# Kernel optimization log

Hardware: AMD Instinct MI355X
Metric: run time of the kernel (lower is better)

## Reference

```python
import jax, jax.numpy as jnp
import numpy as np


def setup_inputs() -> dict:
    key = jax.random.key(0)
    k1, k2, k3, k4, k5 = jax.random.split(key, 5)
    NNZ = 1_600_000
    N, IN, OUT = 8192, 4096, 4096
    vals = jax.random.normal(k1, (NNZ,), dtype=jnp.float32)
    rows = jax.random.randint(k2, (NNZ,), 0, N, dtype=jnp.int32)
    cols = jax.random.randint(k3, (NNZ,), 0, IN, dtype=jnp.int32)
    # kaiming_uniform-ish init scale for weight, uniform bias
    bound_w = jnp.sqrt(1.0 / IN)
    weight = jax.random.uniform(k4, (OUT, IN), dtype=jnp.float32, minval=-bound_w, maxval=bound_w)
    bias = jax.random.uniform(k5, (OUT,), dtype=jnp.float32, minval=-bound_w, maxval=bound_w)
    return {"vals": vals, "rows": rows, "cols": cols, "weight": weight, "bias": bias, "n_rows": N}


def reference(vals, rows, cols, weight, bias, n_rows):
    """Sparse COO [n_rows, in_features] @ weight.T + bias (torch.sparse.addmm).

    Densify via scatter-add (COO semantics: duplicate indices accumulate),
    then a single dense GEMM which dominates the cost.
    """
    in_features = weight.shape[1]
    dense = jnp.zeros((n_rows, in_features), dtype=vals.dtype).at[rows, cols].add(vals)
    return dense @ weight.T + bias  # [n_rows, out_features]
```

## Files before the change

kernel.cpp:

```cpp
#include <hip/hip_runtime.h>

typedef __attribute__((ext_vector_type(8)))  __bf16 bf16x8;
typedef __attribute__((ext_vector_type(4)))  float  f32x4;
typedef __attribute__((ext_vector_type(8)))  unsigned short u16x8;

__device__ inline unsigned short f2bf(float f) {
    unsigned int u = __float_as_uint(f);
    u += 0x7FFFu + ((u >> 16) & 1u);
    return (unsigned short)(u >> 16);
}

__global__ __launch_bounds__(256) void scatter_bf16(
        const float* __restrict__ vals,
        const int* __restrict__ rows,
        const int* __restrict__ cols,
        unsigned short* __restrict__ Ab,
        int nnz, int in_f) {
    int i = blockIdx.x * blockDim.x + threadIdx.x;
    if (i >= nnz) return;
    float v = vals[i];
    size_t idx = (size_t)rows[i] * in_f + cols[i];
    unsigned int* word = (unsigned int*)(Ab + (idx & ~(size_t)1));
    unsigned int sh = (unsigned int)(idx & 1) * 16u;
    unsigned int old = *word, assumed;
    do {
        assumed = old;
        unsigned int cur = (assumed >> sh) & 0xFFFFu;
        float f = __uint_as_float(cur << 16) + v;
        unsigned int nb = f2bf(f);
        unsigned int repl = (assumed & ~(0xFFFFu << sh)) | (nb << sh);
        old = atomicCAS(word, assumed, repl);
    } while (old != assumed);
}

__global__ __launch_bounds__(256) void cvt_kernel(
        const float* __restrict__ src,
        unsigned short* __restrict__ dst,
        long n) {
    long i = ((long)blockIdx.x * blockDim.x + threadIdx.x) * 8;
    if (i + 8 <= n) {
        f32x4 a = *(const f32x4*)(src + i);
        f32x4 b = *(const f32x4*)(src + i + 4);
        u16x8 o;
        o[0] = f2bf(a[0]); o[1] = f2bf(a[1]); o[2] = f2bf(a[2]); o[3] = f2bf(a[3]);
        o[4] = f2bf(b[0]); o[5] = f2bf(b[1]); o[6] = f2bf(b[2]); o[7] = f2bf(b[3]);
        *(u16x8*)(dst + i) = o;
    }
}


__device__ __forceinline__ bf16x8 read_frag(const unsigned short* slab, int row, int g) {
    return *(const bf16x8*)(slab + row * 32 + ((g ^ (row & 3)) << 3));
}

__device__ __forceinline__ void stage_slab(const unsigned short* __restrict__ G,
                                           int grow0, int K, int kelem,
                                           unsigned short* slab, int tid) {
    const int lane = tid & 63, wv = tid >> 6;
    #pragma unroll
    for (int j = 0; j < 2; ++j) {
        int u = wv * 128 + j * 64 + lane;
        int row = u >> 2, slot = u & 3;
        const unsigned short* g = G + (size_t)(grow0 + row) * K
                                    + (kelem + ((slot ^ (row & 3)) << 3));
        unsigned short* l = slab + (wv * 128 + j * 64) * 8;
        __builtin_amdgcn_global_load_lds(
            (const __attribute__((address_space(1))) void*)g,
            (__attribute__((address_space(3))) void*)l, 16, 0, 0);
    }
}

__global__ __launch_bounds__(512, 2) void gemm_bt_bias(
    const unsigned short* __restrict__ A,
    const unsigned short* __restrict__ B,
    const float* __restrict__ bias,
    float* __restrict__ C,
    int M, int N, int K)
{
    __shared__ unsigned short sA[2][2][8192];
    __shared__ unsigned short sB[2][2][8192];

    const int tid  = threadIdx.x;
    const int lane = tid & 63;
    const int wave = tid >> 6;
    const int wm = (wave >> 2) * 128;
    const int wn = (wave & 3) * 64;
    const int r15 = lane & 15;
    const int g   = lane >> 4;

    const int nbx = gridDim.x;
    const int nwg = gridDim.x * gridDim.y;
    int flat = blockIdx.y * gridDim.x + blockIdx.x;
    int rid = (nwg & 7) ? flat : ((flat & 7) * (nwg >> 3) + (flat >> 3));
    const int bm = (rid / nbx) * 256;
    const int bn = (rid % nbx) * 256;

    f32x4 acc[8][4];
    #pragma unroll
    for (int i = 0; i < 8; ++i)
        #pragma unroll
        for (int jg = 0; jg < 4; ++jg)
            #pragma unroll
            for (int r = 0; r < 4; ++r) acc[i][jg][r] = 0.f;

    stage_slab(A, bm, K, 0,       &sA[0][0][0], tid);
    stage_slab(B, bn, K, 0,       &sB[0][0][0], tid);
    stage_slab(A, bm, K, 32,      &sA[0][1][0], tid);
    stage_slab(B, bn, K, 32,      &sB[0][1][0], tid);
    stage_slab(A, bm, K, 64,      &sA[1][0][0], tid);
    stage_slab(B, bn, K, 64,      &sB[1][0][0], tid);
    asm volatile("s_waitcnt vmcnt(8)" ::: "memory");
    __builtin_amdgcn_s_barrier();

    const int nt = K >> 6;
    for (int t = 0; t < nt; ++t) {
        const int cur = t & 1, nxt = cur ^ 1;
        const int t1k = ((t + 1 < nt) ? t + 1 : 0) << 6;
        const int t2k = ((t + 2 < nt) ? t + 2 : 0) << 6;
        const unsigned short* sAc0 = &sA[cur][0][0];
        const unsigned short* sAc1 = &sA[cur][1][0];
        const unsigned short* sBc0 = &sB[cur][0][0];
        const unsigned short* sBc1 = &sB[cur][1][0];

        bf16x8 a[8], b[2];

        #pragma unroll
        for (int i = 0; i < 8; ++i) a[i] = read_frag(sAc0, wm + i * 16 + r15, g);
        b[0] = read_frag(sBc0, wn + r15, g);
        b[1] = read_frag(sBc0, wn + 16 + r15, g);
        stage_slab(A, bm, K, t1k + 32, &sA[nxt][1][0], tid);
        __builtin_amdgcn_s_barrier();
        asm volatile("s_waitcnt lgkmcnt(0)" ::: "memory");
        __builtin_amdgcn_s_setprio(1);
        #pragma unroll
        for (int i = 0; i < 8; ++i) {
            acc[i][0] = __builtin_amdgcn_mfma_f32_16x16x32_bf16(a[i], b[0], acc[i][0], 0, 0, 0);
            acc[i][1] = __builtin_amdgcn_mfma_f32_16x16x32_bf16(a[i], b[1], acc[i][1], 0, 0, 0);
        }
        __builtin_amdgcn_s_setprio(0);
        __builtin_amdgcn_s_barrier();

        b[0] = read_frag(sBc0, wn + 32 + r15, g);
        b[1] = read_frag(sBc0, wn + 48 + r15, g);
        stage_slab(B, bn, K, t1k + 32, &sB[nxt][1][0], tid);
        __builtin_amdgcn_s_barrier();
        asm volatile("s_waitcnt lgkmcnt(0)" ::: "memory");
        __builtin_amdgcn_s_setprio(1);
        #pragma unroll
        for (int i = 0; i < 8; ++i) {
            acc[i][2] = __builtin_amdgcn_mfma_f32_16x16x32_bf16(a[i], b[0], acc[i][2], 0, 0, 0);
            acc[i][3] = __builtin_amdgcn_mfma_f32_16x16x32_bf16(a[i], b[1], acc[i][3], 0, 0, 0);
        }
        __builtin_amdgcn_s_setprio(0);
        asm volatile("s_waitcnt vmcnt(8)" ::: "memory");
        __builtin_amdgcn_s_barrier();

        #pragma unroll
        for (int i = 0; i < 8; ++i) a[i] = read_frag(sAc1, wm + i * 16 + r15, g);
        b[0] = read_frag(sBc1, wn + r15, g);
        b[1] = read_frag(sBc1, wn + 16 + r15, g);
        stage_slab(A, bm, K, t2k, &sA[cur][0][0], tid);
        __builtin_amdgcn_s_barrier();
        asm volatile("s_waitcnt lgkmcnt(0)" ::: "memory");
        __builtin_amdgcn_s_setprio(1);
        #pragma unroll
        for (int i = 0; i < 8; ++i) {
            acc[i][0] = __builtin_amdgcn_mfma_f32_16x16x32_bf16(a[i], b[0], acc[i][0], 0, 0, 0);
            acc[i][1] = __builtin_amdgcn_mfma_f32_16x16x32_bf16(a[i], b[1], acc[i][1], 0, 0, 0);
        }
        __builtin_amdgcn_s_setprio(0);
        __builtin_amdgcn_s_barrier();

        b[0] = read_frag(sBc1, wn + 32 + r15, g);
        b[1] = read_frag(sBc1, wn + 48 + r15, g);
        stage_slab(B, bn, K, t2k, &sB[cur][0][0], tid);
        __builtin_amdgcn_s_barrier();
        asm volatile("s_waitcnt lgkmcnt(0)" ::: "memory");
        __builtin_amdgcn_s_setprio(1);
        #pragma unroll
        for (int i = 0; i < 8; ++i) {
            acc[i][2] = __builtin_amdgcn_mfma_f32_16x16x32_bf16(a[i], b[0], acc[i][2], 0, 0, 0);
            acc[i][3] = __builtin_amdgcn_mfma_f32_16x16x32_bf16(a[i], b[1], acc[i][3], 0, 0, 0);
        }
        __builtin_amdgcn_s_setprio(0);
        asm volatile("s_waitcnt vmcnt(8)" ::: "memory");
        __builtin_amdgcn_s_barrier();
    }

    #pragma unroll
    for (int jg = 0; jg < 4; ++jg) {
        int col = bn + wn + jg * 16 + r15;
        float bv = bias[col];
        #pragma unroll
        for (int i = 0; i < 8; ++i) {
            int rbase = bm + wm + i * 16 + g * 4;
            #pragma unroll
            for (int r = 0; r < 4; ++r) {
                __builtin_nontemporal_store(acc[i][jg][r] + bv,
                                            &C[(size_t)(rbase + r) * N + col]);
            }
        }
    }
}

extern "C" void kernel_launch(void* const* d_in, const int* in_sizes, int n_in,
                              void* d_out, int out_size, void* d_ws, size_t ws_size,
                              hipStream_t stream) {
    const float* vals   = (const float*)d_in[0];
    const int*   rows   = (const int*)d_in[1];
    const int*   cols   = (const int*)d_in[2];
    const float* weight = (const float*)d_in[3];
    const float* bias   = (const float*)d_in[4];

    const int NNZ = in_sizes[0];
    const int OUT = in_sizes[4];
    const int IN  = in_sizes[3] / OUT;
    const int M   = out_size / OUT;

    unsigned short* Ab = (unsigned short*)d_ws;
    size_t abBytes = (size_t)M * IN * sizeof(unsigned short);
    unsigned short* Wb = (unsigned short*)((char*)d_ws + abBytes);

    hipMemsetAsync(Ab, 0, abBytes, stream);

    scatter_bf16<<<(NNZ + 255) / 256, 256, 0, stream>>>(vals, rows, cols, Ab, NNZ, IN);

    {
        long nW = (long)OUT * IN;
        cvt_kernel<<<(int)((nW / 8 + 255) / 256), 256, 0, stream>>>(weight, Wb, nW);
    }

    dim3 grid(OUT / 256, M / 256);
    gemm_bt_bias<<<grid, 512, 0, stream>>>(Ab, Wb, bias, (float*)d_out, M, OUT, IN);
}
```

Before: 535.8 us.

## Fuse scatter and weight cast, use bf16 atomic add, restructure GEMM LDS staging

```diff
diff --git a/kernel.cpp b/kernel.cpp
--- a/kernel.cpp
+++ b/kernel.cpp
@@ -10,16 +10,40 @@
     return (unsigned short)(u >> 16);
 }
 
-__global__ __launch_bounds__(256) void scatter_bf16(
+__global__ __launch_bounds__(256) void scatter_cvt(
         const float* __restrict__ vals,
         const int* __restrict__ rows,
         const int* __restrict__ cols,
         unsigned short* __restrict__ Ab,
-        int nnz, int in_f) {
-    int i = blockIdx.x * blockDim.x + threadIdx.x;
+        int nnz, int in_f,
+        const float* __restrict__ wsrc,
+        unsigned short* __restrict__ wdst,
+        long nW, int cvtBlocks) {
+    if ((int)blockIdx.x < cvtBlocks) {
+        long i = ((long)blockIdx.x * 256 + threadIdx.x) * 8;
+        if (i + 8 <= nW) {
+            f32x4 a = *(const f32x4*)(wsrc + i);
+            f32x4 b = *(const f32x4*)(wsrc + i + 4);
+            u16x8 o;
+            o[0] = f2bf(a[0]); o[1] = f2bf(a[1]); o[2] = f2bf(a[2]); o[3] = f2bf(a[3]);
+            o[4] = f2bf(b[0]); o[5] = f2bf(b[1]); o[6] = f2bf(b[2]); o[7] = f2bf(b[3]);
+            *(u16x8*)(wdst + i) = o;
+        }
+        return;
+    }
+    int i = ((int)blockIdx.x - cvtBlocks) * 256 + threadIdx.x;
     if (i >= nnz) return;
     float v = vals[i];
     size_t idx = (size_t)rows[i] * in_f + cols[i];
+#if __has_builtin(__builtin_amdgcn_global_atomic_fadd_v2bf16)
+    typedef __attribute__((ext_vector_type(2))) short s16x2;
+    unsigned short hv = f2bf(v);
+    s16x2 add;
+    add[0] = (idx & 1) ? (short)0 : (short)hv;
+    add[1] = (idx & 1) ? (short)hv : (short)0;
+    __builtin_amdgcn_global_atomic_fadd_v2bf16(
+        (__attribute__((address_space(1))) s16x2*)(Ab + (idx & ~(size_t)1)), add);
+#else
     unsigned int* word = (unsigned int*)(Ab + (idx & ~(size_t)1));
     unsigned int sh = (unsigned int)(idx & 1) * 16u;
     unsigned int old = *word, assumed;
@@ -31,39 +55,26 @@
         unsigned int repl = (assumed & ~(0xFFFFu << sh)) | (nb << sh);
         old = atomicCAS(word, assumed, repl);
     } while (old != assumed);
-}
-
-__global__ __launch_bounds__(256) void cvt_kernel(
-        const float* __restrict__ src,
-        unsigned short* __restrict__ dst,
-        long n) {
-    long i = ((long)blockIdx.x * blockDim.x + threadIdx.x) * 8;
-    if (i + 8 <= n) {
-        f32x4 a = *(const f32x4*)(src + i);
-        f32x4 b = *(const f32x4*)(src + i + 4);
-        u16x8 o;
-        o[0] = f2bf(a[0]); o[1] = f2bf(a[1]); o[2] = f2bf(a[2]); o[3] = f2bf(a[3]);
-        o[4] = f2bf(b[0]); o[5] = f2bf(b[1]); o[6] = f2bf(b[2]); o[7] = f2bf(b[3]);
-        *(u16x8*)(dst + i) = o;
-    }
-}
-
-
-__device__ __forceinline__ bf16x8 read_frag(const unsigned short* slab, int row, int g) {
-    return *(const bf16x8*)(slab + row * 32 + ((g ^ (row & 3)) << 3));
-}
-
-__device__ __forceinline__ void stage_slab(const unsigned short* __restrict__ G,
-                                           int grow0, int K, int kelem,
-                                           unsigned short* slab, int tid) {
+#endif
+}
+
+
+__device__ __forceinline__ bf16x8 read_frag(const unsigned short* hb, int rowl, int c) {
+    int cs = c ^ ((rowl >> 1) & 2);
+    return *(const bf16x8*)(hb + rowl * 64 + (cs << 3));
+}
+
+__device__ __forceinline__ void stage_half(const unsigned short* __restrict__ G,
+                                           int grow0, int K, int kbase,
+                                           unsigned short* hb, int tid) {
     const int lane = tid & 63, wv = tid >> 6;
     #pragma unroll
     for (int j = 0; j < 2; ++j) {
-        int u = wv * 128 + j * 64 + lane;
-        int row = u >> 2, slot = u & 3;
-        const unsigned short* g = G + (size_t)(grow0 + row) * K
-                                    + (kelem + ((slot ^ (row & 3)) << 3));
-        unsigned short* l = slab + (wv * 128 + j * 64) * 8;
+        int u = j * 512 + wv * 64 + lane;
+        int rowl = u >> 3;
+        int c = (u & 7) ^ ((u >> 4) & 2);
+        const unsigned short* g = G + (size_t)(grow0 + rowl) * K + kbase + c * 8;
+        unsigned short* l = hb + (size_t)(j * 512 + wv * 64) * 8;
         __builtin_amdgcn_global_load_lds(
             (const __attribute__((address_space(1))) void*)g,
             (__attribute__((address_space(3))) void*)l, 16, 0, 0);
@@ -87,6 +98,9 @@
     const int wn = (wave & 3) * 64;
     const int r15 = lane & 15;
     const int g   = lane >> 4;
+    const int ah  = wm >> 7;
+    const int bh  = wn >> 7;
+    const int bro = wn & 64;
 
     const int nbx = gridDim.x;
     const int nwg = gridDim.x * gridDim.y;
@@ -103,13 +117,13 @@
             #pragma unroll
             for (int r = 0; r < 4; ++r) acc[i][jg][r] = 0.f;
 
-    stage_slab(A, bm, K, 0,       &sA[0][0][0], tid);
-    stage_slab(B, bn, K, 0,       &sB[0][0][0], tid);
-    stage_slab(A, bm, K, 32,      &sA[0][1][0], tid);
-    stage_slab(B, bn, K, 32,      &sB[0][1][0], tid);
-    stage_slab(A, bm, K, 64,      &sA[1][0][0], tid);
-    stage_slab(B, bn, K, 64,      &sB[1][0][0], tid);
-    asm volatile("s_waitcnt vmcnt(8)" ::: "memory");
+    stage_half(A, bm,       K, 0,  &sA[0][0][0], tid);
+    stage_half(A, bm + 128, K, 0,  &sA[0][1][0], tid);
+    stage_half(B, bn,       K, 0,  &sB[0][0][0], tid);
+    stage_half(B, bn + 128, K, 0,  &sB[0][1][0], tid);
+    stage_half(A, bm,       K, 64, &sA[1][0][0], tid);
+    stage_half(A, bm + 128, K, 64, &sA[1][1][0], tid);
+    asm volatile("s_waitcnt vmcnt(4)" ::: "memory");
     __builtin_amdgcn_s_barrier();
 
     const int nt = K >> 6;
@@ -117,75 +131,77 @@
         const int cur = t & 1, nxt = cur ^ 1;
         const int t1k = ((t + 1 < nt) ? t + 1 : 0) << 6;
         const int t2k = ((t + 2 < nt) ? t + 2 : 0) << 6;
-        const unsigned short* sAc0 = &sA[cur][0][0];
-        const unsigned short* sAc1 = &sA[cur][1][0];
-        const unsigned short* sBc0 = &sB[cur][0][0];
-        const unsigned short* sBc1 = &sB[cur][1][0];
-
-        bf16x8 a[8], b[2];
-
-        #pragma unroll
-        for (int i = 0; i < 8; ++i) a[i] = read_frag(sAc0, wm + i * 16 + r15, g);
-        b[0] = read_frag(sBc0, wn + r15, g);
-        b[1] = read_frag(sBc0, wn + 16 + r15, g);
-        stage_slab(A, bm, K, t1k + 32, &sA[nxt][1][0], tid);
-        __builtin_amdgcn_s_barrier();
-        asm volatile("s_waitcnt lgkmcnt(0)" ::: "memory");
-        __builtin_amdgcn_s_setprio(1);
-        #pragma unroll
-        for (int i = 0; i < 8; ++i) {
-            acc[i][0] = __builtin_amdgcn_mfma_f32_16x16x32_bf16(a[i], b[0], acc[i][0], 0, 0, 0);
-            acc[i][1] = __builtin_amdgcn_mfma_f32_16x16x32_bf16(a[i], b[1], acc[i][1], 0, 0, 0);
-        }
-        __builtin_amdgcn_s_setprio(0);
-        __builtin_amdgcn_s_barrier();
-
-        b[0] = read_frag(sBc0, wn + 32 + r15, g);
-        b[1] = read_frag(sBc0, wn + 48 + r15, g);
-        stage_slab(B, bn, K, t1k + 32, &sB[nxt][1][0], tid);
-        __builtin_amdgcn_s_barrier();
-        asm volatile("s_waitcnt lgkmcnt(0)" ::: "memory");
-        __builtin_amdgcn_s_setprio(1);
-        #pragma unroll
-        for (int i = 0; i < 8; ++i) {
-            acc[i][2] = __builtin_amdgcn_mfma_f32_16x16x32_bf16(a[i], b[0], acc[i][2], 0, 0, 0);
-            acc[i][3] = __builtin_amdgcn_mfma_f32_16x16x32_bf16(a[i], b[1], acc[i][3], 0, 0, 0);
-        }
-        __builtin_amdgcn_s_setprio(0);
-        asm volatile("s_waitcnt vmcnt(8)" ::: "memory");
-        __builtin_amdgcn_s_barrier();
-
-        #pragma unroll
-        for (int i = 0; i < 8; ++i) a[i] = read_frag(sAc1, wm + i * 16 + r15, g);
-        b[0] = read_frag(sBc1, wn + r15, g);
-        b[1] = read_frag(sBc1, wn + 16 + r15, g);
-        stage_slab(A, bm, K, t2k, &sA[cur][0][0], tid);
-        __builtin_amdgcn_s_barrier();
-        asm volatile("s_waitcnt lgkmcnt(0)" ::: "memory");
-        __builtin_amdgcn_s_setprio(1);
-        #pragma unroll
-        for (int i = 0; i < 8; ++i) {
-            acc[i][0] = __builtin_amdgcn_mfma_f32_16x16x32_bf16(a[i], b[0], acc[i][0], 0, 0, 0);
-            acc[i][1] = __builtin_amdgcn_mfma_f32_16x16x32_bf16(a[i], b[1], acc[i][1], 0, 0, 0);
-        }
-        __builtin_amdgcn_s_setprio(0);
-        __builtin_amdgcn_s_barrier();
-
-        b[0] = read_frag(sBc1, wn + 32 + r15, g);
-        b[1] = read_frag(sBc1, wn + 48 + r15, g);
-        stage_slab(B, bn, K, t2k, &sB[cur][0][0], tid);
-        __builtin_amdgcn_s_barrier();
-        asm volatile("s_waitcnt lgkmcnt(0)" ::: "memory");
-        __builtin_amdgcn_s_setprio(1);
-        #pragma unroll
-        for (int i = 0; i < 8; ++i) {
-            acc[i][2] = __builtin_amdgcn_mfma_f32_16x16x32_bf16(a[i], b[0], acc[i][2], 0, 0, 0);
-            acc[i][3] = __builtin_amdgcn_mfma_f32_16x16x32_bf16(a[i], b[1], acc[i][3], 0, 0, 0);
-        }
-        __builtin_amdgcn_s_setprio(0);
-        asm volatile("s_waitcnt vmcnt(8)" ::: "memory");
-        __builtin_amdgcn_s_barrier();
-    }
+        const unsigned short* sAh = &sA[cur][ah][0];
+        const unsigned short* sBh = &sB[cur][bh][0];
+
+        bf16x8 a[8], b0, b1;
+
+        #pragma unroll
+        for (int i = 0; i < 8; ++i) a[i] = read_frag(sAh, i * 16 + r15, g);
+        b0 = read_frag(sBh, bro + r15, g);
+        b1 = read_frag(sBh, bro + 16 + r15, g);
+        stage_half(B, bn,       K, t1k, &sB[nxt][0][0], tid);
+        stage_half(B, bn + 128, K, t1k, &sB[nxt][1][0], tid);
+        __builtin_amdgcn_s_barrier();
+        asm volatile("s_waitcnt lgkmcnt(0)" ::: "memory");
+        __builtin_amdgcn_sched_barrier(0);
+        __builtin_amdgcn_s_setprio(1);
+        #pragma unroll
+        for (int i = 0; i < 8; ++i) {
+            acc[i][0] = __builtin_amdgcn_mfma_f32_16x16x32_bf16(a[i], b0, acc[i][0], 0, 0, 0);
+            acc[i][1] = __builtin_amdgcn_mfma_f32_16x16x32_bf16(a[i], b1, acc[i][1], 0, 0, 0);
+        }
+        __builtin_amdgcn_s_setprio(0);
+        __builtin_amdgcn_s_barrier();
+
+        b0 = read_frag(sBh, bro + 32 + r15, g);
+        b1 = read_frag(sBh, bro + 48 + r15, g);
+        __builtin_amdgcn_s_barrier();
+        asm volatile("s_waitcnt lgkmcnt(0)" ::: "memory");
+        __builtin_amdgcn_sched_barrier(0);
+        __builtin_amdgcn_s_setprio(1);
+        #pragma unroll
+        for (int i = 0; i < 8; ++i) {
+            acc[i][2] = __builtin_amdgcn_mfma_f32_16x16x32_bf16(a[i], b0, acc[i][2], 0, 0, 0);
+            acc[i][3] = __builtin_amdgcn_mfma_f32_16x16x32_bf16(a[i], b1, acc[i][3], 0, 0, 0);
+        }
+        __builtin_amdgcn_s_setprio(0);
+        __builtin_amdgcn_s_barrier();
+
+        #pragma unroll
+        for (int i = 0; i < 8; ++i) a[i] = read_frag(sAh, i * 16 + r15, 4 + g);
+        b0 = read_frag(sBh, bro + r15, 4 + g);
+        b1 = read_frag(sBh, bro + 16 + r15, 4 + g);
+        __builtin_amdgcn_s_barrier();
+        asm volatile("s_waitcnt lgkmcnt(0)" ::: "memory");
+        __builtin_amdgcn_sched_barrier(0);
+        __builtin_amdgcn_s_setprio(1);
+        #pragma unroll
+        for (int i = 0; i < 8; ++i) {
+            acc[i][0] = __builtin_amdgcn_mfma_f32_16x16x32_bf16(a[i], b0, acc[i][0], 0, 0, 0);
+            acc[i][1] = __builtin_amdgcn_mfma_f32_16x16x32_bf16(a[i], b1, acc[i][1], 0, 0, 0);
+        }
+        __builtin_amdgcn_s_setprio(0);
+        __builtin_amdgcn_s_barrier();
+
+        b0 = read_frag(sBh, bro + 32 + r15, 4 + g);
+        b1 = read_frag(sBh, bro + 48 + r15, 4 + g);
+        stage_half(A, bm,       K, t2k, &sA[cur][0][0], tid);
+        stage_half(A, bm + 128, K, t2k, &sA[cur][1][0], tid);
+        __builtin_amdgcn_s_barrier();
+        asm volatile("s_waitcnt lgkmcnt(0)" ::: "memory");
+        __builtin_amdgcn_sched_barrier(0);
+        __builtin_amdgcn_s_setprio(1);
+        #pragma unroll
+        for (int i = 0; i < 8; ++i) {
+            acc[i][2] = __builtin_amdgcn_mfma_f32_16x16x32_bf16(a[i], b0, acc[i][2], 0, 0, 0);
+            acc[i][3] = __builtin_amdgcn_mfma_f32_16x16x32_bf16(a[i], b1, acc[i][3], 0, 0, 0);
+        }
+        __builtin_amdgcn_s_setprio(0);
+        asm volatile("s_waitcnt vmcnt(4)" ::: "memory");
+        __builtin_amdgcn_s_barrier();
+    }
+    asm volatile("s_waitcnt vmcnt(0)" ::: "memory");
 
     #pragma unroll
     for (int jg = 0; jg < 4; ++jg) {
@@ -223,11 +239,12 @@
 
     hipMemsetAsync(Ab, 0, abBytes, stream);
 
-    scatter_bf16<<<(NNZ + 255) / 256, 256, 0, stream>>>(vals, rows, cols, Ab, NNZ, IN);
-
     {
         long nW = (long)OUT * IN;
-        cvt_kernel<<<(int)((nW / 8 + 255) / 256), 256, 0, stream>>>(weight, Wb, nW);
+        int cvtBlocks = (int)((nW / 8 + 255) / 256);
+        int scBlocks  = (NNZ + 255) / 256;
+        scatter_cvt<<<cvtBlocks + scBlocks, 256, 0, stream>>>(
+            vals, rows, cols, Ab, NNZ, IN, weight, Wb, nW, cvtBlocks);
     }
 
     dim3 grid(OUT / 256, M / 256);
```

New measurement: 528.9 us. No clear change (-1.3%).
